# Optimization experiments

Hardware: AMD Instinct MI355X
Metric: run time of the kernel (lower is better)

The kernel has to match this reference:

```python
import jax, jax.numpy as jnp
import numpy as np
from jax import lax

DT = 0.01
DT_SCALE = 1.0


def setup_inputs() -> dict:
    key = jax.random.key(0)
    ks = jax.random.split(key, 5)
    B, D, R = 32768, 256, 32
    return {
        "x": jax.random.normal(ks[0], (B, D), dtype=jnp.float32),
        "v": jax.random.normal(ks[1], (B, D), dtype=jnp.float32),
        "force": jax.random.normal(ks[2], (B, D), dtype=jnp.float32),
        "U": jax.random.normal(ks[3], (D, R), dtype=jnp.float32) * 0.1,
        "W": jax.random.normal(ks[4], (R, D), dtype=jnp.float32) * 0.1,
        "steps": 8,
    }


def reference(x, v, force, U, W, steps):
    # Low-rank quadratic-form christoffel: gamma(v) = ((v @ U)**2) @ W.
    # Friction mu = 0.0 (christoffel returns a single tensor in the original).
    eff_dt = DT * DT_SCALE
    h = 0.5 * eff_dt
    mu = 0.0

    def christoffel(vv):
        return jnp.einsum("br,rd->bd", jnp.einsum("bd,dr->br", vv, U) ** 2, W)

    def step(carry, _):
        cx, cv = carry
        gamma = christoffel(cv)
        v_half = (cv + h * (force - gamma)) / (1.0 + h * mu)
        cx = cx + eff_dt * v_half
        # topology 0 -> Euclidean boundary: identity
        gamma_half = christoffel(v_half)
        cv = (v_half + h * (force - gamma_half)) / (1.0 + h * mu)
        return (cx, cv), None

    (cx, cv), _ = lax.scan(step, (x, v), None, length=steps)
    return cx, cv
```

## Files before the change

kernel.cpp:

```cpp
#include <hip/hip_runtime.h>

typedef __attribute__((ext_vector_type(4))) float f32x4;
typedef __attribute__((ext_vector_type(8))) short bf16x8;

constexpr float EFF_DT = 0.01f;
constexpr float HH     = 0.005f;
constexpr float INV_DT = 100.0f;

__device__ inline short f2bf(float x){
    union{float f;unsigned u;}c; c.f=x;
    unsigned r=c.u+0x7FFFu+((c.u>>16)&1u);
    return (short)(r>>16);
}
__device__ inline unsigned cvtpk(float lo,float hi){
    unsigned r; asm("v_cvt_pk_bf16_f32 %0, %1, %2":"=v"(r):"v"(lo),"v"(hi)); return r;
}
__device__ inline float ubflo(unsigned u){union{unsigned x;float f;}c;c.x=u<<16;return c.f;}
__device__ inline float ubfhi(unsigned u){union{unsigned x;float f;}c;c.x=u&0xffff0000u;return c.f;}

union VP4 { unsigned u[4]; bf16x8 h; };

__global__ __launch_bounds__(256,2) void leapfrog_v13(
    const float* __restrict__ x_in, const float* __restrict__ v_in,
    const float* __restrict__ f_in, const float* __restrict__ Ug,
    const float* __restrict__ Wg, const int* __restrict__ steps_p,
    float* __restrict__ out)
{
    __shared__ __align__(16) char lds[81920];
    short* WF = (short*)lds;

    const int tid=threadIdx.x, w=tid>>6, lane=tid&63, g=lane>>4, c=lane&15;
    const int R0 = blockIdx.x*64 + w*16;
    const int gb = (R0+c)*256 + g*4;
    const int BD = 32768*256;
    float* xw = (float*)(lds + 16384 + w*16384);

    f32x4 vv[16];
    unsigned fpk[16][2];
    bf16x8 uf[2][8];

    #pragma unroll
    for(int dt=0;dt<16;++dt) vv[dt] = *(const f32x4*)&v_in[gb+dt*16];

    #pragma unroll
    for(int rt=0;rt<2;++rt){
        #pragma unroll
        for(int cc=0;cc<8;++cc){
            bf16x8 e;
            #pragma unroll
            for(int j=0;j<8;++j){
                const int kk = ((j>>2)<<4) + g*4 + (j&3);
                e[j] = f2bf(Ug[(cc*32+kk)*32 + rt*16 + c]);
            }
            uf[rt][cc] = e;
        }
    }
    #pragma unroll
    for(int i=0;i<4;++i){
        const int t = w*4+i;
        bf16x8 e;
        #pragma unroll
        for(int j=0;j<8;++j){
            const int kk = ((j>>2)<<4) + g*4 + (j&3);
            e[j] = f2bf(-HH * Wg[kk*256 + t*16 + c]);
        }
        *(bf16x8*)&WF[t*512 + lane*8] = e;
    }
    #pragma unroll
    for(int dt=0;dt<16;++dt){
        f32x4 ff = *(const f32x4*)&f_in[gb+dt*16];
        fpk[dt][0]=cvtpk(HH*ff[0],HH*ff[1]);
        fpk[dt][1]=cvtpk(HH*ff[2],HH*ff[3]);
    }
    #pragma unroll
    for(int dt=0;dt<16;++dt){
        f32x4 xx = *(const f32x4*)&x_in[gb+dt*16];
        f32x4 xs; xs[0]=INV_DT*xx[0]; xs[1]=INV_DT*xx[1];
        xs[2]=INV_DT*xx[2]; xs[3]=INV_DT*xx[3];
        *(f32x4*)&xw[dt*256 + lane*4] = xs;
    }
    __syncthreads();

    const int nsteps = *steps_p;
    const f32x4 zero = {0.f,0.f,0.f,0.f};

#define PHASE_AB(ACCX, STX, STV) do { \
    f32x4 a00=zero,a01=zero,a10=zero,a11=zero; \
    __builtin_amdgcn_s_setprio(1); \
    _Pragma("unroll") \
    for(int cc=0;cc<8;++cc){ \
        VP4 vp; \
        vp.u[0]=cvtpk(vv[2*cc][0],  vv[2*cc][1]); \
        vp.u[1]=cvtpk(vv[2*cc][2],  vv[2*cc][3]); \
        vp.u[2]=cvtpk(vv[2*cc+1][0],vv[2*cc+1][1]); \
        vp.u[3]=cvtpk(vv[2*cc+1][2],vv[2*cc+1][3]); \
        if(cc&1){ a01=__builtin_amdgcn_mfma_f32_16x16x32_bf16(uf[0][cc],vp.h,a01,0,0,0); \
                  a11=__builtin_amdgcn_mfma_f32_16x16x32_bf16(uf[1][cc],vp.h,a11,0,0,0); } \
        else    { a00=__builtin_amdgcn_mfma_f32_16x16x32_bf16(uf[0][cc],vp.h,a00,0,0,0); \
                  a10=__builtin_amdgcn_mfma_f32_16x16x32_bf16(uf[1][cc],vp.h,a10,0,0,0); } \
    } \
    { \
        float t00=a00[0]+a01[0], t01=a00[1]+a01[1], t02=a00[2]+a01[2], t03=a00[3]+a01[3]; \
        float t10=a10[0]+a11[0], t11=a10[1]+a11[1], t12=a10[2]+a11[2], t13=a10[3]+a11[3]; \
        VP4 t2; \
        t2.u[0]=cvtpk(t00*t00, t01*t01); \
        t2.u[1]=cvtpk(t02*t02, t03*t03); \
        t2.u[2]=cvtpk(t10*t10, t11*t11); \
        t2.u[3]=cvtpk(t12*t12, t13*t13); \
        __builtin_amdgcn_s_setprio(0); \
        _Pragma("unroll") \
        for(int dt=0;dt<16;++dt){ \
            bf16x8 wf=*(bf16x8*)&WF[dt*512 + lane*8]; \
            const unsigned f0=fpk[dt][0], f1=fpk[dt][1]; \
            f32x4 cin; \
            cin[0]=vv[dt][0]+ubflo(f0); \
            cin[1]=vv[dt][1]+ubfhi(f0); \
            cin[2]=vv[dt][2]+ubflo(f1); \
            cin[3]=vv[dt][3]+ubfhi(f1); \
            f32x4 nv=__builtin_amdgcn_mfma_f32_16x16x32_bf16(wf,t2.h,cin,0,0,0); \
            vv[dt]=nv; \
            if(ACCX){ \
                f32x4* xp=(f32x4*)&xw[dt*256 + lane*4]; \
                f32x4 xv=*xp; \
                xv[0]+=nv[0]; xv[1]+=nv[1]; xv[2]+=nv[2]; xv[3]+=nv[3]; \
                if(STX){ \
                    f32x4 xo; \
                    xo[0]=EFF_DT*xv[0]; xo[1]=EFF_DT*xv[1]; \
                    xo[2]=EFF_DT*xv[2]; xo[3]=EFF_DT*xv[3]; \
                    *(f32x4*)&out[gb+dt*16] = xo; \
                }else{ \
                    *xp = xv; \
                } \
            } \
            if(STV){ \
                *(f32x4*)&out[BD+gb+dt*16] = nv; \
            } \
        } \
    } \
} while(0)

    for(int s=0;s<nsteps-1;++s){
        PHASE_AB(1,0,0);
        PHASE_AB(0,0,0);
    }
    PHASE_AB(1,1,0);
    PHASE_AB(0,0,1);
#undef PHASE_AB
}

extern "C" void kernel_launch(void* const* d_in, const int* in_sizes, int n_in,
                              void* d_out, int out_size, void* d_ws, size_t ws_size,
                              hipStream_t stream) {
    (void)in_sizes; (void)n_in; (void)d_ws; (void)ws_size; (void)out_size;
    const float* x_in = (const float*)d_in[0];
    const float* v_in = (const float*)d_in[1];
    const float* f_in = (const float*)d_in[2];
    const float* Ug   = (const float*)d_in[3];
    const float* Wg   = (const float*)d_in[4];
    const int*   st   = (const int*)d_in[5];
    float* out = (float*)d_out;

    dim3 grid(32768/64), block(256);
    hipLaunchKernelGGL(leapfrog_v13, grid, block, 0, stream,
                       x_in, v_in, f_in, Ug, Wg, st, out);
}
```

Measured before the change: 43.44 us.

## Keep x displacement accumulator in bf16 registers, move force to LDS

The x accumulator moves out of LDS (previously 16KB per wave of fp32, read and written every other phase) into packed bf16 registers that hold only the summed velocity increments. x_in is now read once at the end and combined with an fma. The packed force terms move from registers into LDS to free register space, and total LDS shrinks from 80KB to 48KB. The bf16 accumulation of the x displacement loses precision over the steps, and the force is now read from LDS in every phase.

```diff
diff --git a/kernel.cpp b/kernel.cpp
--- a/kernel.cpp
+++ b/kernel.cpp
@@ -2,10 +2,10 @@
 
 typedef __attribute__((ext_vector_type(4))) float f32x4;
 typedef __attribute__((ext_vector_type(8))) short bf16x8;
+typedef __attribute__((ext_vector_type(2))) unsigned u32x2;
 
 constexpr float EFF_DT = 0.01f;
 constexpr float HH     = 0.005f;
-constexpr float INV_DT = 100.0f;
 
 __device__ inline short f2bf(float x){
     union{float f;unsigned u;}c; c.f=x;
@@ -20,23 +20,23 @@
 
 union VP4 { unsigned u[4]; bf16x8 h; };
 
-__global__ __launch_bounds__(256,2) void leapfrog_v13(
+__global__ __launch_bounds__(256,2) void leapfrog_v15(
     const float* __restrict__ x_in, const float* __restrict__ v_in,
     const float* __restrict__ f_in, const float* __restrict__ Ug,
     const float* __restrict__ Wg, const int* __restrict__ steps_p,
     float* __restrict__ out)
 {
-    __shared__ __align__(16) char lds[81920];
+    __shared__ __align__(16) char lds[49152];
     short* WF = (short*)lds;
+    u32x2* FPW = (u32x2*)(lds + 16384 + (threadIdx.x>>6)*8192);
 
     const int tid=threadIdx.x, w=tid>>6, lane=tid&63, g=lane>>4, c=lane&15;
     const int R0 = blockIdx.x*64 + w*16;
     const int gb = (R0+c)*256 + g*4;
     const int BD = 32768*256;
-    float* xw = (float*)(lds + 16384 + w*16384);
 
     f32x4 vv[16];
-    unsigned fpk[16][2];
+    unsigned xpk[16][2];
     bf16x8 uf[2][8];
 
     #pragma unroll
@@ -69,22 +69,18 @@
     #pragma unroll
     for(int dt=0;dt<16;++dt){
         f32x4 ff = *(const f32x4*)&f_in[gb+dt*16];
-        fpk[dt][0]=cvtpk(HH*ff[0],HH*ff[1]);
-        fpk[dt][1]=cvtpk(HH*ff[2],HH*ff[3]);
-    }
-    #pragma unroll
-    for(int dt=0;dt<16;++dt){
-        f32x4 xx = *(const f32x4*)&x_in[gb+dt*16];
-        f32x4 xs; xs[0]=INV_DT*xx[0]; xs[1]=INV_DT*xx[1];
-        xs[2]=INV_DT*xx[2]; xs[3]=INV_DT*xx[3];
-        *(f32x4*)&xw[dt*256 + lane*4] = xs;
+        u32x2 p;
+        p.x = cvtpk(HH*ff[0],HH*ff[1]);
+        p.y = cvtpk(HH*ff[2],HH*ff[3]);
+        FPW[dt*64 + lane] = p;
+        xpk[dt][0]=0u; xpk[dt][1]=0u;
     }
     __syncthreads();
 
     const int nsteps = *steps_p;
     const f32x4 zero = {0.f,0.f,0.f,0.f};
 
-#define PHASE_AB(ACCX, STX, STV) do { \
+#define PHASE_AB(ACCX, STV) do { \
     f32x4 a00=zero,a01=zero,a10=zero,a11=zero; \
     __builtin_amdgcn_s_setprio(1); \
     _Pragma("unroll") \
@@ -111,26 +107,18 @@
         _Pragma("unroll") \
         for(int dt=0;dt<16;++dt){ \
             bf16x8 wf=*(bf16x8*)&WF[dt*512 + lane*8]; \
-            const unsigned f0=fpk[dt][0], f1=fpk[dt][1]; \
+            const u32x2 fp = FPW[dt*64 + lane]; \
             f32x4 cin; \
-            cin[0]=vv[dt][0]+ubflo(f0); \
-            cin[1]=vv[dt][1]+ubfhi(f0); \
-            cin[2]=vv[dt][2]+ubflo(f1); \
-            cin[3]=vv[dt][3]+ubfhi(f1); \
+            cin[0]=vv[dt][0]+ubflo(fp.x); \
+            cin[1]=vv[dt][1]+ubfhi(fp.x); \
+            cin[2]=vv[dt][2]+ubflo(fp.y); \
+            cin[3]=vv[dt][3]+ubfhi(fp.y); \
             f32x4 nv=__builtin_amdgcn_mfma_f32_16x16x32_bf16(wf,t2.h,cin,0,0,0); \
             vv[dt]=nv; \
             if(ACCX){ \
-                f32x4* xp=(f32x4*)&xw[dt*256 + lane*4]; \
-                f32x4 xv=*xp; \
-                xv[0]+=nv[0]; xv[1]+=nv[1]; xv[2]+=nv[2]; xv[3]+=nv[3]; \
-                if(STX){ \
-                    f32x4 xo; \
-                    xo[0]=EFF_DT*xv[0]; xo[1]=EFF_DT*xv[1]; \
-                    xo[2]=EFF_DT*xv[2]; xo[3]=EFF_DT*xv[3]; \
-                    *(f32x4*)&out[gb+dt*16] = xo; \
-                }else{ \
-                    *xp = xv; \
-                } \
+                const unsigned x0=xpk[dt][0], x1=xpk[dt][1]; \
+                xpk[dt][0]=cvtpk(ubflo(x0)+nv[0], ubfhi(x0)+nv[1]); \
+                xpk[dt][1]=cvtpk(ubflo(x1)+nv[2], ubfhi(x1)+nv[3]); \
             } \
             if(STV){ \
                 *(f32x4*)&out[BD+gb+dt*16] = nv; \
@@ -140,11 +128,24 @@
 } while(0)
 
     for(int s=0;s<nsteps-1;++s){
-        PHASE_AB(1,0,0);
-        PHASE_AB(0,0,0);
+        PHASE_AB(1,0);
+        PHASE_AB(0,0);
     }
-    PHASE_AB(1,1,0);
-    PHASE_AB(0,0,1);
+    PHASE_AB(1,0);
+
+    #pragma unroll
+    for(int dt=0;dt<16;++dt){
+        f32x4 xx = *(const f32x4*)&x_in[gb+dt*16];
+        const unsigned x0=xpk[dt][0], x1=xpk[dt][1];
+        f32x4 xo;
+        xo[0]=fmaf(EFF_DT, ubflo(x0), xx[0]);
+        xo[1]=fmaf(EFF_DT, ubfhi(x0), xx[1]);
+        xo[2]=fmaf(EFF_DT, ubflo(x1), xx[2]);
+        xo[3]=fmaf(EFF_DT, ubfhi(x1), xx[3]);
+        *(f32x4*)&out[gb+dt*16] = xo;
+    }
+
+    PHASE_AB(0,1);
 #undef PHASE_AB
 }
 
@@ -161,6 +162,6 @@
     float* out = (float*)d_out;
 
     dim3 grid(32768/64), block(256);
-    hipLaunchKernelGGL(leapfrog_v13, grid, block, 0, stream,
+    hipLaunchKernelGGL(leapfrog_v15, grid, block, 0, stream,
                        x_in, v_in, f_in, Ug, Wg, st, out);
 }
```

Result: slower. 46.73 us (+7.6%).
